# Kernel optimization log

Measured on AMD Instinct MI355X. Metric: run time of the kernel, lower is better.

Reference implementation:

```python
import jax, jax.numpy as jnp
import numpy as np
from jax import lax

B, S, H = 4, 2048, 2048
E, TOPK = 32, 8
I_MOE = 768
I_SHARED = 4096


def setup_inputs() -> dict:
    key = jax.random.key(0)
    ks = jax.random.split(key, 9)
    sc = 0.02
    return {
        "hidden_states": jax.random.normal(ks[0], (B, S, H), jnp.float32),
        "gate_w": jax.random.normal(ks[1], (H, E), jnp.float32) * sc,
        "Wg": jax.random.normal(ks[2], (E, H, I_MOE), jnp.float32) * sc,
        "Wu": jax.random.normal(ks[3], (E, H, I_MOE), jnp.float32) * sc,
        "Wd": jax.random.normal(ks[4], (E, I_MOE, H), jnp.float32) * sc,
        "Sg": jax.random.normal(ks[5], (H, I_SHARED), jnp.float32) * sc,
        "Su": jax.random.normal(ks[6], (H, I_SHARED), jnp.float32) * sc,
        "Sd": jax.random.normal(ks[7], (I_SHARED, H), jnp.float32) * sc,
        "shared_gate_w": jax.random.normal(ks[8], (H, 1), jnp.float32) * sc,
    }


def reference(hidden_states, gate_w, Wg, Wu, Wd, Sg, Su, Sd, shared_gate_w):
    b, s, h = hidden_states.shape
    x = hidden_states.reshape(-1, h)                      # [T, H]
    T = x.shape[0]

    # router: softmax in fp32, top-k, renormalize (norm_topk_prob=True)
    router_logits = x @ gate_w                            # [T, E]
    probs = jax.nn.softmax(router_logits.astype(jnp.float32), axis=-1)
    topk_w, topk_idx = lax.top_k(probs, TOPK)             # [T, K]
    topk_w = topk_w / jnp.sum(topk_w, axis=-1, keepdims=True)
    topk_w = topk_w.astype(x.dtype)

    # dense combine weights: zero for unrouted (token, expert) pairs
    combine = jnp.zeros((T, E), x.dtype).at[jnp.arange(T)[:, None], topk_idx].add(topk_w)

    # scan over experts: SwiGLU MLP, weighted accumulate (scatter-combine)
    def step(acc, packed):
        wg, wu, wd, cw = packed                           # cw: [T]
        hmid = jax.nn.silu(x @ wg) * (x @ wu)             # [T, I_MOE]
        return acc + (hmid @ wd) * cw[:, None], None

    moe_out, _ = lax.scan(step, jnp.zeros_like(x), (Wg, Wu, Wd, combine.T))

    # shared expert with sigmoid gate
    shared = (jax.nn.silu(x @ Sg) * (x @ Su)) @ Sd        # [T, H]
    shared = jax.nn.sigmoid(x @ shared_gate_w) * shared

    final = (moe_out + shared).reshape(b, s, h)
    return final, router_logits
```

## Files before the change

kernel.cpp:

```cpp
#include <hip/hip_runtime.h>
#include <stdint.h>

#define T_TOK 8192
#define HD    2048
#define NE    32
#define KTOP  8
#define IM    768
#define IS    4096

typedef unsigned short u16;
typedef __attribute__((ext_vector_type(8))) short bf16x8;
typedef __attribute__((ext_vector_type(4))) float f32x4;

__device__ __forceinline__ u16 f2b(float f) {
    union { float f; unsigned u; } c; c.f = f;
    unsigned u = c.u;
    return (u16)((u + 0x7FFFu + ((u >> 16) & 1u)) >> 16);
}

__global__ __launch_bounds__(256) void router_kernel(
    const float* __restrict__ x, const float* __restrict__ gate_w,
    const float* __restrict__ sgw, float* __restrict__ logits_out,
    u16* __restrict__ xb, float* __restrict__ sgvals,
    int* __restrict__ topk_idx, float* __restrict__ topk_w,
    int* __restrict__ counts)
{
    const int t = blockIdx.x, tid = threadIdx.x;
    __shared__ __align__(16) float xrow[HD];
    __shared__ float red[256];
    __shared__ float sh_logit[NE];

    const float4* xr = (const float4*)(x + (size_t)t * HD);
    float4 v0 = xr[tid * 2], v1 = xr[tid * 2 + 1];
    *(float4*)&xrow[tid * 8]     = v0;
    *(float4*)&xrow[tid * 8 + 4] = v1;
    ushort4 p0; p0.x = f2b(v0.x); p0.y = f2b(v0.y); p0.z = f2b(v0.z); p0.w = f2b(v0.w);
    ushort4 p1; p1.x = f2b(v1.x); p1.y = f2b(v1.y); p1.z = f2b(v1.z); p1.w = f2b(v1.w);
    *(ushort4*)&xb[(size_t)t * HD + tid * 8]     = p0;
    *(ushort4*)&xb[(size_t)t * HD + tid * 8 + 4] = p1;
    __syncthreads();

    const int e = tid & 31, seg = tid >> 5;
    float acc = 0.f;
    const float* gwp = gate_w + e;
    for (int j = seg * 256; j < seg * 256 + 256; ++j)
        acc = fmaf(xrow[j], gwp[j * NE], acc);
    red[tid] = acc;
    __syncthreads();
    if (tid < NE) {
        float l = 0.f;
        #pragma unroll
        for (int s = 0; s < 8; ++s) l += red[s * 32 + tid];
        sh_logit[tid] = l;
        logits_out[(size_t)t * NE + tid] = l;
    }
    __syncthreads();

    float sacc = v0.x * sgw[tid * 8 + 0] + v0.y * sgw[tid * 8 + 1] + v0.z * sgw[tid * 8 + 2] + v0.w * sgw[tid * 8 + 3]
               + v1.x * sgw[tid * 8 + 4] + v1.y * sgw[tid * 8 + 5] + v1.z * sgw[tid * 8 + 6] + v1.w * sgw[tid * 8 + 7];
    red[tid] = sacc;
    __syncthreads();
    if (tid < 128) red[tid] += red[tid + 128];
    __syncthreads();
    if (tid < 64) {
        float s2 = red[tid] + red[tid + 64];
        #pragma unroll
        for (int off = 32; off; off >>= 1) s2 += __shfl_xor(s2, off, 64);
        if (tid == 0) sgvals[t] = 1.f / (1.f + __expf(-s2));

        float v = (tid < NE) ? sh_logit[tid] : -3.0e38f;
        float m = v;
        #pragma unroll
        for (int off = 32; off; off >>= 1) m = fmaxf(m, __shfl_xor(m, off, 64));
        float p = __expf(v - m);
        if (tid >= NE) p = 0.f;
        float ssum = p;
        #pragma unroll
        for (int off = 32; off; off >>= 1) ssum += __shfl_xor(ssum, off, 64);
        float myp = p / ssum;

        float selv[KTOP]; int seli[KTOP];
        float sumtop = 0.f;
        #pragma unroll
        for (int k = 0; k < KTOP; ++k) {
            float bv = myp; int bi = tid;
            #pragma unroll
            for (int off = 32; off; off >>= 1) {
                float ov = __shfl_xor(bv, off, 64);
                int   oi = __shfl_xor(bi, off, 64);
                if (ov > bv || (ov == bv && oi < bi)) { bv = ov; bi = oi; }
            }
            selv[k] = bv; seli[k] = bi; sumtop += bv;
            if (tid == bi) myp = -1.f;
        }
        if (tid == 0) {
            #pragma unroll
            for (int k = 0; k < KTOP; ++k) {
                topk_idx[(size_t)t * KTOP + k] = seli[k];
                topk_w[(size_t)t * KTOP + k]   = selv[k] / sumtop;
                atomicAdd(&counts[seli[k]], 1);
            }
        }
    }
}

__global__ void offsets_kernel(const int* __restrict__ counts,
                               int* __restrict__ offsets, int* __restrict__ cursor)
{
    if (threadIdx.x == 0) {
        int a = 0;
        for (int e = 0; e < NE; ++e) { offsets[e] = a; cursor[e] = a; a += counts[e]; }
    }
}

__global__ __launch_bounds__(256) void scatter_kernel(
    const int* __restrict__ topk_idx, const float* __restrict__ topk_w,
    int* __restrict__ cursor, int* __restrict__ token_list, float* __restrict__ weight_list)
{
    int i = blockIdx.x * 256 + threadIdx.x;
    int e = topk_idx[i];
    int pos = atomicAdd(&cursor[e], 1);
    token_list[pos]  = i >> 3;
    weight_list[pos] = topk_w[i];
}

template<int MODE>
__global__ __launch_bounds__(256, 2) void gemm_k(
    const u16* __restrict__ Asrc, const float* __restrict__ B0g,
    const float* __restrict__ B1g, u16* __restrict__ outb,
    float* __restrict__ outf, const float* __restrict__ scale,
    const int* __restrict__ token_list, const int* __restrict__ counts,
    const int* __restrict__ offsets)
{
    constexpr bool DUAL   = (MODE == 0 || MODE == 2);
    constexpr bool EXPERT = (MODE >= 2);
    constexpr int KTOT = (MODE == 0 || MODE == 2) ? HD : (MODE == 1 ? IS : IM);
    constexpr int NTOT = (MODE == 0) ? IS : (MODE == 2 ? IM : HD);
    constexpr int LDA  = (MODE == 0 || MODE == 2) ? HD : (MODE == 1 ? IS : IM);

    const int tid = threadIdx.x;
    const int ex  = blockIdx.z;
    const int n_e = EXPERT ? counts[ex]  : T_TOK;
    const int off = EXPERT ? offsets[ex] : 0;
    const int m0  = blockIdx.y * 128;
    if (m0 >= n_e) return;
    const int n0 = blockIdx.x * 128;

    const float* B0 = B0g + (EXPERT ? (size_t)ex * KTOT * NTOT : 0);
    const float* B1 = DUAL ? (B1g + (EXPERT ? (size_t)ex * KTOT * NTOT : 0)) : nullptr;

    __shared__ __align__(16) u16 As [128 * 40];
    __shared__ __align__(16) u16 Bs0[128 * 40];
    __shared__ __align__(16) u16 Bs1[DUAL ? 128 * 40 : 8];

    const u16* aptr[2]; int aoff[2];
    #pragma unroll
    for (int i = 0; i < 2; ++i) {
        int c = tid + i * 256;
        int r = c >> 2, xo = c & 3;
        int grow = m0 + r;
        size_t rowidx;
        if (MODE == 0 || MODE == 1) rowidx = (size_t)grow;
        else if (MODE == 2) rowidx = (size_t)((grow < n_e) ? token_list[off + grow] : 0);
        else rowidx = (size_t)(off + grow);
        aptr[i] = Asrc + rowidx * LDA + xo * 8;
        aoff[i] = r * 40 + xo * 8;
    }

    const int kb = tid >> 5, nb = tid & 31;
    const float* bp0 = B0 + (size_t)(kb * 4) * NTOT + n0 + nb * 4;
    const float* bp1 = DUAL ? (B1 + (size_t)(kb * 4) * NTOT + n0 + nb * 4) : nullptr;
    const int bo = (nb * 4) * 40 + kb * 4;

    const int lane = tid & 63, wv = tid >> 6;
    const int wm = (wv >> 1) * 64, wn = (wv & 1) * 64;
    const int lr = lane & 15, quad = lane >> 4;

    f32x4 acc0[4][4], acc1[4][4];
    #pragma unroll
    for (int a = 0; a < 4; ++a)
        #pragma unroll
        for (int b = 0; b < 4; ++b)
            #pragma unroll
            for (int q = 0; q < 4; ++q) { acc0[a][b][q] = 0.f; if (DUAL) acc1[a][b][q] = 0.f; }

    for (int kt = 0; kt < KTOT; kt += 32) {
        uint4 av0 = *(const uint4*)(aptr[0] + kt);
        uint4 av1 = *(const uint4*)(aptr[1] + kt);
        float4 b0v[4], b1v[4];
        #pragma unroll
        for (int i = 0; i < 4; ++i) b0v[i] = *(const float4*)(bp0 + (size_t)(kt + i) * NTOT);
        if (DUAL) {
            #pragma unroll
            for (int i = 0; i < 4; ++i) b1v[i] = *(const float4*)(bp1 + (size_t)(kt + i) * NTOT);
        }
        __syncthreads();
        *(uint4*)&As[aoff[0]] = av0;
        *(uint4*)&As[aoff[1]] = av1;
        {
            const float* f0 = (const float*)b0v;
            #pragma unroll
            for (int j = 0; j < 4; ++j) {
                ushort4 tw; tw.x = f2b(f0[0 * 4 + j]); tw.y = f2b(f0[1 * 4 + j]);
                            tw.z = f2b(f0[2 * 4 + j]); tw.w = f2b(f0[3 * 4 + j]);
                *(ushort4*)&Bs0[bo + j * 40] = tw;
            }
        }
        if (DUAL) {
            const float* f1 = (const float*)b1v;
            #pragma unroll
            for (int j = 0; j < 4; ++j) {
                ushort4 tw; tw.x = f2b(f1[0 * 4 + j]); tw.y = f2b(f1[1 * 4 + j]);
                            tw.z = f2b(f1[2 * 4 + j]); tw.w = f2b(f1[3 * 4 + j]);
                *(ushort4*)&Bs1[bo + j * 40] = tw;
            }
        }
        __syncthreads();

        bf16x8 af[4], bf0[4], bf1[4];
        #pragma unroll
        for (int mt = 0; mt < 4; ++mt) af[mt]  = *(const bf16x8*)&As [(wm + mt * 16 + lr) * 40 + quad * 8];
        #pragma unroll
        for (int nt = 0; nt < 4; ++nt) bf0[nt] = *(const bf16x8*)&Bs0[(wn + nt * 16 + lr) * 40 + quad * 8];
        if (DUAL) {
            #pragma unroll
            for (int nt = 0; nt < 4; ++nt) bf1[nt] = *(const bf16x8*)&Bs1[(wn + nt * 16 + lr) * 40 + quad * 8];
        }
        #pragma unroll
        for (int mt = 0; mt < 4; ++mt)
            #pragma unroll
            for (int nt = 0; nt < 4; ++nt) {
                acc0[mt][nt] = __builtin_amdgcn_mfma_f32_16x16x32_bf16(af[mt], bf0[nt], acc0[mt][nt], 0, 0, 0);
                if (DUAL)
                    acc1[mt][nt] = __builtin_amdgcn_mfma_f32_16x16x32_bf16(af[mt], bf1[nt], acc1[mt][nt], 0, 0, 0);
            }
    }

    if (MODE == 0 || MODE == 2) {
        #pragma unroll
        for (int mt = 0; mt < 4; ++mt)
            #pragma unroll
            for (int rg = 0; rg < 4; ++rg) {
                const int grow = m0 + wm + mt * 16 + quad * 4 + rg;
                if (!EXPERT || grow < n_e) {
                    u16* orow = outb + (size_t)(EXPERT ? (off + grow) : grow) * NTOT + n0 + wn + lr;
                    #pragma unroll
                    for (int nt = 0; nt < 4; ++nt) {
                        float g = acc0[mt][nt][rg];
                        float u = acc1[mt][nt][rg];
                        float sgm = 1.f / (1.f + __expf(-g));
                        orow[nt * 16] = f2b(g * sgm * u);
                    }
                }
            }
    } else if (MODE == 1) {
        #pragma unroll
        for (int mt = 0; mt < 4; ++mt)
            #pragma unroll
            for (int rg = 0; rg < 4; ++rg) {
                const int grow = m0 + wm + mt * 16 + quad * 4 + rg;
                const float s = scale[grow];
                float* orow = outf + (size_t)grow * HD + n0 + wn + lr;
                #pragma unroll
                for (int nt = 0; nt < 4; ++nt) orow[nt * 16] = s * acc0[mt][nt][rg];
            }
    } else {
        #pragma unroll
        for (int mt = 0; mt < 4; ++mt)
            #pragma unroll
            for (int rg = 0; rg < 4; ++rg) {
                const int grow = m0 + wm + mt * 16 + quad * 4 + rg;
                if (grow < n_e) {
                    const int tok   = token_list[off + grow];
                    const float wgt = scale[off + grow];
                    float* orow = outf + (size_t)tok * HD + n0 + wn + lr;
                    #pragma unroll
                    for (int nt = 0; nt < 4; ++nt)
                        unsafeAtomicAdd(&orow[nt * 16], wgt * acc0[mt][nt][rg]);
                }
            }
    }
}

#define OFF_XB      ((size_t)0)
#define OFF_HSH     ((size_t)33554432)
#define OFF_HMID    ((size_t)100663296)
#define OFF_SG      ((size_t)201326592)
#define OFF_TOPKI   ((size_t)201359360)
#define OFF_TOPKW   ((size_t)201621504)
#define OFF_TOKL    ((size_t)201883648)
#define OFF_WGTL    ((size_t)202145792)
#define OFF_COUNTS  ((size_t)202407936)
#define OFF_CURSOR  ((size_t)202408064)
#define OFF_OFFSETS ((size_t)202408192)

extern "C" void kernel_launch(void* const* d_in, const int* in_sizes, int n_in,
                              void* d_out, int out_size, void* d_ws, size_t ws_size,
                              hipStream_t stream)
{
    const float* x   = (const float*)d_in[0];
    const float* gw  = (const float*)d_in[1];
    const float* Wg  = (const float*)d_in[2];
    const float* Wu  = (const float*)d_in[3];
    const float* Wd  = (const float*)d_in[4];
    const float* Sg  = (const float*)d_in[5];
    const float* Su  = (const float*)d_in[6];
    const float* Sd  = (const float*)d_in[7];
    const float* sgw = (const float*)d_in[8];

    float* out        = (float*)d_out;
    float* logits_out = out + (size_t)T_TOK * HD;

    char* ws = (char*)d_ws;
    u16*   xb      = (u16*)  (ws + OFF_XB);
    u16*   hshared = (u16*)  (ws + OFF_HSH);
    u16*   hmid    = (u16*)  (ws + OFF_HMID);
    float* sgvals  = (float*)(ws + OFF_SG);
    int*   topk_i  = (int*)  (ws + OFF_TOPKI);
    float* topk_wv = (float*)(ws + OFF_TOPKW);
    int*   tok_lst = (int*)  (ws + OFF_TOKL);
    float* wgt_lst = (float*)(ws + OFF_WGTL);
    int*   counts  = (int*)  (ws + OFF_COUNTS);
    int*   cursor  = (int*)  (ws + OFF_CURSOR);
    int*   offsets = (int*)  (ws + OFF_OFFSETS);

    hipMemsetAsync(counts, 0, 256, stream);

    router_kernel<<<T_TOK, 256, 0, stream>>>(x, gw, sgw, logits_out, xb, sgvals,
                                             topk_i, topk_wv, counts);
    offsets_kernel<<<1, 64, 0, stream>>>(counts, offsets, cursor);
    scatter_kernel<<<T_TOK * KTOP / 256, 256, 0, stream>>>(topk_i, topk_wv, cursor,
                                                           tok_lst, wgt_lst);

    gemm_k<0><<<dim3(IS / 128, T_TOK / 128, 1), 256, 0, stream>>>(
        xb, Sg, Su, hshared, nullptr, nullptr, nullptr, nullptr, nullptr);
    gemm_k<2><<<dim3(IM / 128, T_TOK / 128, NE), 256, 0, stream>>>(
        xb, Wg, Wu, hmid, nullptr, nullptr, tok_lst, counts, offsets);
    gemm_k<1><<<dim3(HD / 128, T_TOK / 128, 1), 256, 0, stream>>>(
        hshared, Sd, nullptr, nullptr, out, sgvals, nullptr, nullptr, nullptr);
    gemm_k<3><<<dim3(HD / 128, T_TOK / 128, NE), 256, 0, stream>>>(
        hmid, Wd, nullptr, nullptr, out, wgt_lst, tok_lst, counts, offsets);
}
```

Measured before the change: 3.187 ms.

## Pre-pack weights to tiled bf16 and stream tiles via direct global-to-LDS loads

Adds a conversion pass that turns every fp32 weight matrix into bf16 tiles laid out in MFMA fragment order, stored in the workspace. New GEMM kernels then load A and B tiles with global_load_lds into double-buffered shared memory, so the old per-tile fp32 load and convert work inside the GEMM goes away. The conversion runs on every call, reading all weights once in fp32 and writing them once in bf16, and needs a large workspace. If the workspace is too small, the code falls back to the old kernels.

```diff
diff --git a/kernel.cpp b/kernel.cpp
--- a/kernel.cpp
+++ b/kernel.cpp
@@ -16,6 +16,13 @@
     union { float f; unsigned u; } c; c.f = f;
     unsigned u = c.u;
     return (u16)((u + 0x7FFFu + ((u >> 16) & 1u)) >> 16);
+}
+
+__device__ __forceinline__ void gld16(const void* g, void* l) {
+    __builtin_amdgcn_global_load_lds(
+        (__attribute__((address_space(1))) void*)(uintptr_t)g,
+        (__attribute__((address_space(3))) void*)(uint32_t)(uintptr_t)l,
+        16, 0, 0);
 }
 
 __global__ __launch_bounds__(256) void router_kernel(
@@ -124,8 +131,189 @@
     weight_list[pos] = topk_w[i];
 }
 
+__global__ __launch_bounds__(256) void convert_k(
+    const float* __restrict__ W, u16* __restrict__ P, int K, int N)
+{
+    const int n0 = blockIdx.x * 128, kt = blockIdx.y * 32;
+    const size_t eoff = (size_t)blockIdx.z * K * N;
+    const int tid = threadIdx.x;
+    __shared__ __align__(16) float tile[32][128];
+
+    const float* Wb = W + eoff + (size_t)kt * N + n0;
+    #pragma unroll
+    for (int p = 0; p < 4; ++p) {
+        int k = p * 8 + (tid >> 5);
+        *(float4*)&tile[k][(tid & 31) * 4] = *(const float4*)(Wb + (size_t)k * N + (tid & 31) * 4);
+    }
+    __syncthreads();
+
+    const int kblk = K >> 5;
+    u16* Pp = P + eoff + ((size_t)blockIdx.x * kblk + blockIdx.y) * 4096;
+    #pragma unroll
+    for (int s = 0; s < 2; ++s) {
+        int i = s * 256 + tid;
+        int c = i >> 7, n = i & 127;
+        union { u16 us[8]; uint4 v; } pk;
+        #pragma unroll
+        for (int q = 0; q < 8; ++q) pk.us[q] = f2b(tile[c * 8 + q][n]);
+        *(uint4*)&Pp[(size_t)i * 8] = pk.v;
+    }
+}
+
 template<int MODE>
-__global__ __launch_bounds__(256, 2) void gemm_k(
+__global__ __launch_bounds__(256, 2) void gemm_f(
+    const u16* __restrict__ Asrc, const u16* __restrict__ B0p,
+    const u16* __restrict__ B1p, u16* __restrict__ outb,
+    float* __restrict__ outf, const float* __restrict__ scale,
+    const int* __restrict__ token_list, const int* __restrict__ counts,
+    const int* __restrict__ offsets)
+{
+    constexpr bool DUAL   = (MODE == 0 || MODE == 2);
+    constexpr bool EXPERT = (MODE >= 2);
+    constexpr int KTOT = (MODE == 0 || MODE == 2) ? HD : (MODE == 1 ? IS : IM);
+    constexpr int NTOT = (MODE == 0) ? IS : (MODE == 2 ? IM : HD);
+    constexpr int NTIL = DUAL ? 3 : 2;
+    constexpr int NKT  = KTOT / 32;
+
+    const int tid = threadIdx.x;
+    const int ex  = blockIdx.z;
+    const int n_e = EXPERT ? counts[ex]  : T_TOK;
+    const int off = EXPERT ? offsets[ex] : 0;
+    const int m0  = blockIdx.y * 128;
+    if (m0 >= n_e) return;
+    const int n0 = blockIdx.x * 128;
+
+    const size_t ewoff = EXPERT ? (size_t)ex * KTOT * NTOT : 0;
+
+    __shared__ __align__(16) u16 sh[2 * NTIL * 4096];
+
+    const int w = tid >> 6, lane = tid & 63;
+    const int lr = lane & 15, quad = lane >> 4;
+    const int wm = (w >> 1) * 64, wn = (w & 1) * 64;
+    const int ldsw = w * 512;
+
+    const u16* asrc[2];
+    #pragma unroll
+    for (int s = 0; s < 2; ++s) {
+        int i = s * 256 + tid;
+        int c = i >> 7, r = i & 127;
+        int grow = m0 + r;
+        int gc = grow < n_e ? grow : n_e - 1;
+        size_t rowidx;
+        if (MODE == 0 || MODE == 1) rowidx = (size_t)grow;
+        else if (MODE == 2) rowidx = (size_t)token_list[off + gc];
+        else rowidx = (size_t)(off + gc);
+        asrc[s] = Asrc + rowidx * KTOT + c * 8;
+    }
+    const u16* b0 = B0p + ewoff + ((size_t)(n0 >> 7) * NKT) * 4096 + (size_t)tid * 8;
+    const u16* b1 = nullptr;
+    if constexpr (DUAL) b1 = B1p + ewoff + ((size_t)(n0 >> 7) * NKT) * 4096 + (size_t)tid * 8;
+
+    auto stage = [&](int buf, int kt) {
+        u16* A  = sh + (size_t)(buf * NTIL + 0) * 4096;
+        u16* Bt = sh + (size_t)(buf * NTIL + 1) * 4096;
+        #pragma unroll
+        for (int s = 0; s < 2; ++s) {
+            gld16(asrc[s] + kt, A + s * 2048 + ldsw);
+            gld16(b0 + (size_t)(kt >> 5) * 4096 + s * 2048, Bt + s * 2048 + ldsw);
+        }
+        if constexpr (DUAL) {
+            u16* Bu = sh + (size_t)(buf * NTIL + 2) * 4096;
+            #pragma unroll
+            for (int s = 0; s < 2; ++s)
+                gld16(b1 + (size_t)(kt >> 5) * 4096 + s * 2048, Bu + s * 2048 + ldsw);
+        }
+    };
+
+    f32x4 acc0[4][4], acc1[4][4];
+    #pragma unroll
+    for (int a = 0; a < 4; ++a)
+        #pragma unroll
+        for (int b = 0; b < 4; ++b)
+            #pragma unroll
+            for (int q = 0; q < 4; ++q) { acc0[a][b][q] = 0.f; if constexpr (DUAL) acc1[a][b][q] = 0.f; }
+
+    stage(0, 0);
+    int cur = 0;
+    for (int kt = 0; kt < KTOT; kt += 32) {
+        __syncthreads();
+        if (kt + 32 < KTOT) stage(cur ^ 1, kt + 32);
+
+        const u16* A  = sh + (size_t)(cur * NTIL + 0) * 4096;
+        const u16* B0 = sh + (size_t)(cur * NTIL + 1) * 4096;
+
+        bf16x8 af[4], bf0[4], bf1[4];
+        #pragma unroll
+        for (int mt = 0; mt < 4; ++mt)
+            af[mt]  = *(const bf16x8*)&A [quad * 1024 + (wm + mt * 16 + lr) * 8];
+        #pragma unroll
+        for (int nt = 0; nt < 4; ++nt)
+            bf0[nt] = *(const bf16x8*)&B0[quad * 1024 + (wn + nt * 16 + lr) * 8];
+        if constexpr (DUAL) {
+            const u16* B1 = sh + (size_t)(cur * NTIL + 2) * 4096;
+            #pragma unroll
+            for (int nt = 0; nt < 4; ++nt)
+                bf1[nt] = *(const bf16x8*)&B1[quad * 1024 + (wn + nt * 16 + lr) * 8];
+        }
+        #pragma unroll
+        for (int mt = 0; mt < 4; ++mt)
+            #pragma unroll
+            for (int nt = 0; nt < 4; ++nt) {
+                acc0[mt][nt] = __builtin_amdgcn_mfma_f32_16x16x32_bf16(af[mt], bf0[nt], acc0[mt][nt], 0, 0, 0);
+                if constexpr (DUAL)
+                    acc1[mt][nt] = __builtin_amdgcn_mfma_f32_16x16x32_bf16(af[mt], bf1[nt], acc1[mt][nt], 0, 0, 0);
+            }
+        cur ^= 1;
+    }
+
+    if (MODE == 0 || MODE == 2) {
+        #pragma unroll
+        for (int mt = 0; mt < 4; ++mt)
+            #pragma unroll
+            for (int rg = 0; rg < 4; ++rg) {
+                const int grow = m0 + wm + mt * 16 + quad * 4 + rg;
+                if (!EXPERT || grow < n_e) {
+                    u16* orow = outb + (size_t)(EXPERT ? (off + grow) : grow) * NTOT + n0 + wn + lr;
+                    #pragma unroll
+                    for (int nt = 0; nt < 4; ++nt) {
+                        float g = acc0[mt][nt][rg];
+                        float u = acc1[mt][nt][rg];
+                        float sgm = 1.f / (1.f + __expf(-g));
+                        orow[nt * 16] = f2b(g * sgm * u);
+                    }
+                }
+            }
+    } else if (MODE == 1) {
+        #pragma unroll
+        for (int mt = 0; mt < 4; ++mt)
+            #pragma unroll
+            for (int rg = 0; rg < 4; ++rg) {
+                const int grow = m0 + wm + mt * 16 + quad * 4 + rg;
+                const float s = scale[grow];
+                float* orow = outf + (size_t)grow * HD + n0 + wn + lr;
+                #pragma unroll
+                for (int nt = 0; nt < 4; ++nt) orow[nt * 16] = s * acc0[mt][nt][rg];
+            }
+    } else {
+        #pragma unroll
+        for (int mt = 0; mt < 4; ++mt)
+            #pragma unroll
+            for (int rg = 0; rg < 4; ++rg) {
+                const int grow = m0 + wm + mt * 16 + quad * 4 + rg;
+                if (grow < n_e) {
+                    const int tok   = token_list[off + grow];
+                    const float wgt = scale[off + grow];
+                    float* orow = outf + (size_t)tok * HD + n0 + wn + lr;
+                    #pragma unroll
+                    for (int nt = 0; nt < 4; ++nt)
+                        unsafeAtomicAdd(&orow[nt * 16], wgt * acc0[mt][nt][rg]);
+                }
+            }
+    }
+}
+
+template<int MODE>
+__global__ __launch_bounds__(256, 2) void gemm_l(
     const u16* __restrict__ Asrc, const float* __restrict__ B0g,
     const float* __restrict__ B1g, u16* __restrict__ outb,
     float* __restrict__ outf, const float* __restrict__ scale,
@@ -293,6 +481,13 @@
 #define OFF_COUNTS  ((size_t)202407936)
 #define OFF_CURSOR  ((size_t)202408064)
 #define OFF_OFFSETS ((size_t)202408192)
+#define OFF_PWG     ((size_t)202408448)
+#define OFF_PWU     ((size_t)303071744)
+#define OFF_PWD     ((size_t)403735040)
+#define OFF_PSG     ((size_t)504398336)
+#define OFF_PSU     ((size_t)521175552)
+#define OFF_PSD     ((size_t)537952768)
+#define WS_NEED     ((size_t)554729984)
 
 extern "C" void kernel_launch(void* const* d_in, const int* in_sizes, int n_in,
                               void* d_out, int out_size, void* d_ws, size_t ws_size,
@@ -332,12 +527,37 @@
     scatter_kernel<<<T_TOK * KTOP / 256, 256, 0, stream>>>(topk_i, topk_wv, cursor,
                                                            tok_lst, wgt_lst);
 
-    gemm_k<0><<<dim3(IS / 128, T_TOK / 128, 1), 256, 0, stream>>>(
-        xb, Sg, Su, hshared, nullptr, nullptr, nullptr, nullptr, nullptr);
-    gemm_k<2><<<dim3(IM / 128, T_TOK / 128, NE), 256, 0, stream>>>(
-        xb, Wg, Wu, hmid, nullptr, nullptr, tok_lst, counts, offsets);
-    gemm_k<1><<<dim3(HD / 128, T_TOK / 128, 1), 256, 0, stream>>>(
-        hshared, Sd, nullptr, nullptr, out, sgvals, nullptr, nullptr, nullptr);
-    gemm_k<3><<<dim3(HD / 128, T_TOK / 128, NE), 256, 0, stream>>>(
-        hmid, Wd, nullptr, nullptr, out, wgt_lst, tok_lst, counts, offsets);
-}
+    if (ws_size >= WS_NEED) {
+        u16* pWg = (u16*)(ws + OFF_PWG);
+        u16* pWu = (u16*)(ws + OFF_PWU);
+        u16* pWd = (u16*)(ws + OFF_PWD);
+        u16* pSg = (u16*)(ws + OFF_PSG);
+        u16* pSu = (u16*)(ws + OFF_PSU);
+        u16* pSd = (u16*)(ws + OFF_PSD);
+
+        convert_k<<<dim3(IM / 128, HD / 32, NE), 256, 0, stream>>>(Wg, pWg, HD, IM);
+        convert_k<<<dim3(IM / 128, HD / 32, NE), 256, 0, stream>>>(Wu, pWu, HD, IM);
+        convert_k<<<dim3(HD / 128, IM / 32, NE), 256, 0, stream>>>(Wd, pWd, IM, HD);
+        convert_k<<<dim3(IS / 128, HD / 32, 1),  256, 0, stream>>>(Sg, pSg, HD, IS);
+        convert_k<<<dim3(IS / 128, HD / 32, 1),  256, 0, stream>>>(Su, pSu, HD, IS);
+        convert_k<<<dim3(HD / 128, IS / 32, 1),  256, 0, stream>>>(Sd, pSd, IS, HD);
+
+        gemm_f<0><<<dim3(IS / 128, T_TOK / 128, 1), 256, 0, stream>>>(
+            xb, pSg, pSu, hshared, nullptr, nullptr, nullptr, nullptr, nullptr);
+        gemm_f<2><<<dim3(IM / 128, T_TOK / 128, NE), 256, 0, stream>>>(
+            xb, pWg, pWu, hmid, nullptr, nullptr, tok_lst, counts, offsets);
+        gemm_f<1><<<dim3(HD / 128, T_TOK / 128, 1), 256, 0, stream>>>(
+            hshared, pSd, nullptr, nullptr, out, sgvals, nullptr, nullptr, nullptr);
+        gemm_f<3><<<dim3(HD / 128, T_TOK / 128, NE), 256, 0, stream>>>(
+            hmid, pWd, nullptr, nullptr, out, wgt_lst, tok_lst, counts, offsets);
+    } else {
+        gemm_l<0><<<dim3(IS / 128, T_TOK / 128, 1), 256, 0, stream>>>(
+            xb, Sg, Su, hshared, nullptr, nullptr, nullptr, nullptr, nullptr);
+        gemm_l<2><<<dim3(IM / 128, T_TOK / 128, NE), 256, 0, stream>>>(
+            xb, Wg, Wu, hmid, nullptr, nullptr, tok_lst, counts, offsets);
+        gemm_l<1><<<dim3(HD / 128, T_TOK / 128, 1), 256, 0, stream>>>(
+            hshared, Sd, nullptr, nullptr, out, sgvals, nullptr, nullptr, nullptr);
+        gemm_l<3><<<dim3(HD / 128, T_TOK / 128, NE), 256, 0, stream>>>(
+            hmid, Wd, nullptr, nullptr, out, wgt_lst, tok_lst, counts, offsets);
+    }
+}
```

After: 2.830 ms. 1.13x faster.
